# Optimization experiments

Hardware: AMD Instinct MI355X
Metric: run time of the kernel (lower is better)

## Reference

```python
import jax, jax.numpy as jnp
import numpy as np

B, C, H, W = 32, 256, 56, 56
HEADS, M, EXP = 8, 7, 4


def _rel_pos_index(m):
    # Swin V1 pair-wise relative position index, [m*m, m*m] (static)
    coords = np.stack(np.meshgrid(np.arange(m), np.arange(m), indexing='ij'))  # [2,m,m]
    cf = coords.reshape(2, -1)
    rel = (cf[:, :, None] - cf[:, None, :]).transpose(1, 2, 0).copy()
    rel[:, :, 0] += m - 1
    rel[:, :, 1] += m - 1
    rel[:, :, 0] *= 2 * m - 1
    return jnp.asarray(rel.sum(-1))


def setup_inputs():
    key = jax.random.key(0)
    ks = jax.random.split(key, 8)
    s = lambda k, shp: jax.random.normal(k, shp, jnp.float32) * 0.02
    return {
        'x': jax.random.normal(ks[0], (B, C, H, W), jnp.float32),
        'qkv_w': s(ks[1], (3 * C, C)), 'qkv_b': jnp.zeros((3 * C,), jnp.float32),
        'proj_w': s(ks[2], (C, C)), 'proj_b': jnp.zeros((C,), jnp.float32),
        'bias_table': s(ks[3], ((2 * M - 1) * (2 * M - 1), HEADS)),
        'ln1_g': jnp.ones((C,), jnp.float32), 'ln1_b': jnp.zeros((C,), jnp.float32),
        'ln2_g': jnp.ones((C,), jnp.float32), 'ln2_b': jnp.zeros((C,), jnp.float32),
        'w1': s(ks[4], (EXP * C, C)), 'b1': jnp.zeros((EXP * C,), jnp.float32),
        'w2': s(ks[5], (C, EXP * C)), 'b2': jnp.zeros((C,), jnp.float32),
    }


def _layernorm(x, g, b, eps=1e-5):
    mu = x.mean(-1, keepdims=True)
    var = ((x - mu) ** 2).mean(-1, keepdims=True)
    return (x - mu) * jax.lax.rsqrt(var + eps) * g + b


def _block(x, qkv_w, qkv_b, proj_w, proj_b, bias_table,
           ln1_g, ln1_b, ln2_g, ln2_b, w1, b1, w2, b2):
    Bx, Cx, Hx, Wx = x.shape
    N = M * M
    # window partition: [B,C,H,W] -> [B*nw, M*M, C]
    xp = x.reshape(Bx, Cx, Hx // M, M, Wx // M, M)
    xp = xp.transpose(0, 2, 4, 3, 5, 1).reshape(-1, N, Cx)
    B_ = xp.shape[0]
    # relative self-attention (pre-LN)
    h = _layernorm(xp, ln1_g, ln1_b)
    qkv = (h @ qkv_w.T + qkv_b).reshape(B_, N, 3, HEADS, Cx // HEADS)
    qkv = qkv.transpose(2, 0, 3, 1, 4)  # [3,B_,H,N,d]
    q, k, v = qkv[0], qkv[1], qkv[2]
    q = q * (HEADS ** -0.5)  # note: module scales by num_heads**-0.5 (faithful)
    rel_idx = _rel_pos_index(M)
    bias = bias_table[rel_idx.reshape(-1)].reshape(N, N, HEADS).transpose(2, 0, 1)
    attn = jax.nn.softmax(jnp.einsum('bhnd,bhmd->bhnm', q, k) + bias[None], axis=-1)
    out = jnp.einsum('bhnm,bhmd->bhnd', attn, v).transpose(0, 2, 1, 3).reshape(B_, N, Cx)
    xp = xp + (out @ proj_w.T + proj_b)
    # MLP (1x1 Conv1d == pointwise linear), exact GELU as in torch
    h2 = _layernorm(xp, ln2_g, ln2_b)
    h2 = jax.nn.gelu(h2 @ w1.T + b1, approximate=False)
    xp = xp + (h2 @ w2.T + b2)
    # window reverse: [B*nw, M*M, C] -> [B,C,H,W]
    nwh, nww = Hx // M, Wx // M
    y = xp.reshape(Bx, nwh, nww, M, M, Cx).transpose(0, 5, 1, 3, 2, 4).reshape(Bx, Cx, Hx, Wx)
    return y


def reference(x, qkv_w, qkv_b, proj_w, proj_b, bias_table,
              ln1_g, ln1_b, ln2_g, ln2_b, w1, b1, w2, b2):
    return _block(x, qkv_w, qkv_b, proj_w, proj_b, bias_table,
                  ln1_g, ln1_b, ln2_g, ln2_b, w1, b1, w2, b2)
```

## Files before the change

kernel.cpp:

```cpp
#include <hip/hip_runtime.h>
#include <math.h>

#define TB 256

typedef short bf16x8 __attribute__((ext_vector_type(8)));
typedef short s16x4 __attribute__((ext_vector_type(4)));
typedef float f32x4 __attribute__((ext_vector_type(4)));
typedef unsigned short u16;

__device__ __forceinline__ float b2f(u16 u){
  union{unsigned i; float f;} v; v.i=((unsigned)u)<<16; return v.f;
}
__device__ __forceinline__ u16 f2b(float f){
  union{float ff; unsigned i;} v; v.ff=f;
  return (u16)((v.i + 0x7FFFu + ((v.i>>16)&1u))>>16);
}

__device__ __forceinline__ float gelu(float x){
  float z = fabsf(x)*0.70710678118654752f;
  float t = 1.0f/fmaf(0.3275911f, z, 1.0f);
  float p = t*fmaf(t, fmaf(t, fmaf(t, fmaf(t, 1.061405429f, -1.453152027f), 1.421413741f), -0.284496736f), 0.254829592f);
  float erfz = fmaf(-p, __expf(-z*z), 1.0f);
  float s = (x >= 0.f) ? erfz : -erfz;
  return 0.5f*x*(1.0f + s);
}

__global__ void k_prep(const float* __restrict__ qkv_w, const float* __restrict__ proj_w,
                       const float* __restrict__ w1, const float* __restrict__ w2,
                       const float* __restrict__ btab,
                       u16* __restrict__ wq, u16* __restrict__ wp,
                       u16* __restrict__ w1b, u16* __restrict__ w2b,
                       float* __restrict__ biasT){
  int i = blockIdx.x*TB + threadIdx.x;
  if(i < 196608){ wq[i] = f2b(qkv_w[i]); return; }
  i -= 196608;
  if(i < 65536){ wp[i] = f2b(proj_w[i]); return; }
  i -= 65536;
  if(i < 262144){ w1b[i] = f2b(w1[i]); return; }
  i -= 262144;
  if(i < 262144){ w2b[i] = f2b(w2[i]); return; }
  i -= 262144;
  if(i < 32768){
    int h = i>>12, kq = i&4095, k = kq>>6, q = kq&63;
    float v = 0.f;
    if(k<49 && q<49){
      int qi=q/7, qj=q-qi*7, ki=k/7, kj=k-ki*7;
      v = btab[((qi-ki+6)*13 + (qj-kj+6))*8 + h];
    }
    biasT[i] = v;
  }
}

__global__ __launch_bounds__(256) void k_post(const u16* __restrict__ x2lin, float* __restrict__ out){
  __shared__ u16 tile[12544];
  const int bid = blockIdx.x;
  const int bb = bid>>6, wh=(bid>>3)&7, chunk=bid&7;
  const int wb = bb*64 + wh*8;
  for(int e=threadIdx.x; e<12544; e+=256){
    int ww = e/1568, rem = e - ww*1568, r = rem>>5, cc = rem&31;
    tile[cc*392 + ww*49 + r] = x2lin[(size_t)(wb+ww)*12544 + r*256 + chunk*32 + cc];
  }
  __syncthreads();
  for(int idx=threadIdx.x; idx<12544; idx+=256){
    int c = idx/392, rem = idx - c*392, ii = rem/56, w = rem - ii*56;
    int ww = w/7, j = w - ww*7;
    out[((size_t)(bb*256 + chunk*32 + c))*3136 + (size_t)(wh*7+ii)*56 + w]
        = b2f(tile[c*392 + ww*49 + ii*7 + j]);
  }
}

#define QB_OFF  32768
#define KB_OFF  65536
#define VT_OFF  98304
#define XS_OFF  65536
#define BLK_LDS 131072

__global__ __launch_bounds__(1024,2) void k_block(
    const float* __restrict__ x,
    const u16* __restrict__ wqkv,  const float* __restrict__ bqkv,
    const u16* __restrict__ wproj, const float* __restrict__ bproj,
    const float* __restrict__ biasT,
    const float* __restrict__ g1, const float* __restrict__ bt1,
    const u16* __restrict__ w1, const float* __restrict__ b1v,
    const u16* __restrict__ w2, const float* __restrict__ b2v,
    const float* __restrict__ g2, const float* __restrict__ bt2,
    u16* __restrict__ x2lin)
{
  extern __shared__ char lds[];
  const int tid = threadIdx.x;
  const int wv = tid >> 6, l = tid & 63;
  const int lr = l & 15, lg = l >> 4;
  const unsigned swzA = ((unsigned)(lr & 7)) << 4;
  const unsigned swzR = ((unsigned)((lr>>2) & 3)) << 4;
  const int win = ((blockIdx.x & 7) << 8) | (blockIdx.x >> 3);
  const int bb = win >> 6, wh = (win >> 3) & 7, ww = win & 7;
  const float* xwin = x + (size_t)bb*802816 + (size_t)wh*392 + ww*7;

  float* xs = (float*)(lds + XS_OFF);
  {
    const int j = tid & 7, rbase = tid >> 3;
    #pragma unroll
    for(int it=0; it<14; ++it){
      int run = it*128 + rbase;
      int c = run/7, ii = run - (run/7)*7;
      if(j<7) xs[c*53 + ii*7 + j] = xwin[(size_t)c*3136 + ii*56 + j];
    }
  }
  __syncthreads();

  {
    float gg[4], bgm[4];
    #pragma unroll
    for(int k2=0;k2<4;++k2){ gg[k2]=g1[l+64*k2]; bgm[k2]=bt1[l+64*k2]; }
    #pragma unroll
    for(int s=0;s<4;++s){
      int n = wv + s*16;
      if(n<49){
        float xv[4];
        #pragma unroll
        for(int k2=0;k2<4;++k2) xv[k2] = xs[(l+64*k2)*53 + n];
        float sm=0.f, sq=0.f;
        #pragma unroll
        for(int k2=0;k2<4;++k2){ sm+=xv[k2]; sq+=xv[k2]*xv[k2]; }
        #pragma unroll
        for(int off=32;off>=1;off>>=1){ sm+=__shfl_xor(sm,off); sq+=__shfl_xor(sq,off); }
        float mu=sm*(1.f/256.f), var=sq*(1.f/256.f)-mu*mu;
        float rs=rsqrtf(var+1e-5f);
        #pragma unroll
        for(int k2=0;k2<4;++k2){
          int c=l+64*k2;
          unsigned off2 = (((unsigned)n)*512u + ((unsigned)c)*2u) ^ (((unsigned)(n&7))<<4);
          *(u16*)(lds + off2) = f2b((xv[k2]-mu)*rs*gg[k2]+bgm[k2]);
        }
      }
    }
  }
  for(int m=tid; m<3840; m+=1024) *(u16*)(lds + 49*512 + m*2) = 0;
  __syncthreads();

  for(int m=tid; m<3840; m+=1024){
    int hd = m/480, rm = m - hd*480;
    int d = rm/15, r = 49 + (rm - (rm/15)*15);
    *(u16*)(lds + ((unsigned)(VT_OFF + hd*4096 + d*128 + r*2) ^ ((((unsigned)d)&7u)<<4))) = 0;
  }

  for(int ct=wv; ct<48; ct+=16){
    const u16* wrow = wqkv + ((size_t)(ct*16+lr))*256 + lg*8;
    f32x4 acc[4];
    #pragma unroll
    for(int rt=0;rt<4;++rt) acc[rt]=(f32x4){0.f,0.f,0.f,0.f};
    #pragma unroll
    for(int kq=0; kq<4; ++kq){
      bf16x8 bfr[2];
      #pragma unroll
      for(int k=0;k<2;++k) bfr[k] = *(const bf16x8*)(wrow + kq*64 + k*32);
      #pragma unroll
      for(int rt=0; rt<4; ++rt){
        #pragma unroll
        for(int k=0;k<2;++k){
          bf16x8 afr = *(const bf16x8*)(lds + ((((unsigned)(rt*16+lr))*512u + (unsigned)((kq*2+k)*64+lg*16)) ^ swzA));
          acc[rt] = __builtin_amdgcn_mfma_f32_16x16x32_bf16(bfr[k], afr, acc[rt], 0,0,0);
        }
      }
    }
    f32x4 b4 = *(const f32x4*)(bqkv + ct*16 + lg*4);
    const int s3 = ct>>4, hd = (ct>>1)&7, db = (ct&1)*16 + lg*4;
    #pragma unroll
    for(int rt=0; rt<4; ++rt){
      const int r = rt*16 + lr;
      if(r<49){
        if(s3==0){
          s16x4 pk;
          #pragma unroll
          for(int i=0;i<4;++i) pk[i] = (short)f2b((acc[rt][i]+b4[i])*0.35355339059327373f);
          *(s16x4*)(lds + ((unsigned)(QB_OFF + hd*4096 + r*64 + db*2) ^ swzR)) = pk;
        } else if(s3==1){
          s16x4 pk;
          #pragma unroll
          for(int i=0;i<4;++i) pk[i] = (short)f2b(acc[rt][i]+b4[i]);
          *(s16x4*)(lds + ((unsigned)(KB_OFF + hd*4096 + r*64 + db*2) ^ swzR)) = pk;
        } else {
          #pragma unroll
          for(int i=0;i<4;++i)
            *(u16*)(lds + ((unsigned)(VT_OFF + hd*4096 + (db+i)*128 + r*2) ^ ((((unsigned)(db+i))&7u)<<4))) = f2b(acc[rt][i]+b4[i]);
        }
      }
    }
  }
  __syncthreads();

  {
    const int h = wv & 7, half = wv >> 3;
    s16x4 pkk[2][4];
    #pragma unroll
    for(int j=0;j<2;++j){
      const int qt = half*2 + j;
      bf16x8 qf = *(const bf16x8*)(lds + ((unsigned)(QB_OFF + h*4096 + (qt*16+lr)*64 + lg*16) ^ swzR));
      f32x4 st[4];
      #pragma unroll
      for(int kt=0;kt<4;++kt){
        bf16x8 kfk = *(const bf16x8*)(lds + ((unsigned)(KB_OFF + h*4096 + (kt*16+lr)*64 + lg*16) ^ swzR));
        f32x4 bini;
        #pragma unroll
        for(int i=0;i<4;++i) bini[i] = biasT[h*4096 + (kt*16+lg*4+i)*64 + qt*16+lr];
        st[kt] = __builtin_amdgcn_mfma_f32_16x16x32_bf16(kfk, qf, bini, 0,0,0);
      }
      #pragma unroll
      for(int i=0;i<4;++i)
        if(!(lg==0 && i==0)) st[3][i] = -1e30f;

      float mx = -1e30f;
      #pragma unroll
      for(int kt=0;kt<4;++kt)
        #pragma unroll
        for(int i=0;i<4;++i) mx = fmaxf(mx, st[kt][i]);
      mx = fmaxf(mx, __shfl_xor(mx,16));
      mx = fmaxf(mx, __shfl_xor(mx,32));
      float su = 0.f;
      #pragma unroll
      for(int kt=0;kt<4;++kt)
        #pragma unroll
        for(int i=0;i<4;++i){ float p = __expf(st[kt][i]-mx); st[kt][i]=p; su+=p; }
      su += __shfl_xor(su,16);
      su += __shfl_xor(su,32);
      float inv = 1.f/su;
      #pragma unroll
      for(int kt=0;kt<4;++kt)
        #pragma unroll
        for(int i=0;i<4;++i) pkk[j][kt][i] = (short)f2b(st[kt][i]*inv);
    }
    __syncthreads();

    char* Pb = lds + h*8192;
    #pragma unroll
    for(int j=0;j<2;++j){
      const unsigned rq = (unsigned)((half*2+j)*16 + lr);
      #pragma unroll
      for(int kt=0;kt<4;++kt)
        *(s16x4*)(Pb + ((rq*128u + (unsigned)(kt*32+lg*8)) ^ swzA)) = pkk[j][kt];
    }
    #pragma unroll
    for(int j=0;j<2;++j){
      const int qt = half*2 + j;
      const unsigned rq = (unsigned)(qt*16 + lr);
      bf16x8 pf0 = *(const bf16x8*)(Pb + ((rq*128u + (unsigned)(lg*16)) ^ swzA));
      bf16x8 pf1 = *(const bf16x8*)(Pb + ((rq*128u + (unsigned)(64+lg*16)) ^ swzA));
      #pragma unroll
      for(int dt=0;dt<2;++dt){
        bf16x8 vf0 = *(const bf16x8*)(lds + ((unsigned)(VT_OFF + h*4096 + (dt*16+lr)*128 + lg*16) ^ swzA));
        bf16x8 vf1 = *(const bf16x8*)(lds + ((unsigned)(VT_OFF + h*4096 + (dt*16+lr)*128 + 64+lg*16) ^ swzA));
        f32x4 o = {0.f,0.f,0.f,0.f};
        o = __builtin_amdgcn_mfma_f32_16x16x32_bf16(pf0, vf0, o, 0,0,0);
        o = __builtin_amdgcn_mfma_f32_16x16x32_bf16(pf1, vf1, o, 0,0,0);
        #pragma unroll
        for(int i=0;i<4;++i)
          *(u16*)(lds + ((unsigned)(KB_OFF + h*4096 + (qt*16+lg*4+i)*64 + (dt*16+lr)*2) ^ (((unsigned)lg)<<4))) = f2b(o[i]);
      }
    }
  }
  __syncthreads();

  {
    const int c = wv*16 + lr;
    const u16* wrow = wproj + (size_t)c*256 + lg*8;
    const float pbP = bproj[c];
    f32x4 acc[4];
    #pragma unroll
    for(int mt=0;mt<4;++mt) acc[mt]=(f32x4){0.f,0.f,0.f,0.f};
    #pragma unroll
    for(int kq=0; kq<4; ++kq){
      bf16x8 bfrP[2];
      #pragma unroll
      for(int k=0;k<2;++k) bfrP[k] = *(const bf16x8*)(wrow + kq*64 + k*32);
      #pragma unroll
      for(int mt=0; mt<4; ++mt){
        #pragma unroll
        for(int k=0;k<2;++k){
          bf16x8 afr = *(const bf16x8*)(lds + ((unsigned)(KB_OFF + (kq*2+k)*4096 + (mt*16+lr)*64 + lg*16) ^ swzR));
          acc[mt] = __builtin_amdgcn_mfma_f32_16x16x32_bf16(afr, bfrP[k], acc[mt], 0,0,0);
        }
      }
    }
    #pragma unroll
    for(int mt=0; mt<4; ++mt){
      #pragma unroll
      for(int i=0;i<4;++i){
        int r = mt*16 + lg*4 + i;
        if(r<49){
          int ii=r/7, jj=r-ii*7;
          float val = acc[mt][i] + pbP + xwin[(size_t)c*3136 + ii*56 + jj];
          *(u16*)(lds + ((((unsigned)r)*512u + ((unsigned)c)*2u) ^ (((unsigned)(r&7))<<4))) = f2b(val);
        }
      }
    }
  }
  for(int m=tid; m<3840; m+=1024){
    int r = 49 + (m>>8), c = m & 255;
    *(u16*)(lds + ((((unsigned)r)*512u + ((unsigned)c)*2u) ^ (((unsigned)(r&7))<<4))) = 0;
  }
  __syncthreads();

  {
    float gg[4], bb2[4];
    #pragma unroll
    for(int k2=0;k2<4;++k2){ gg[k2]=g2[l+64*k2]; bb2[k2]=bt2[l+64*k2]; }
    #pragma unroll
    for(int rr=0; rr<4; ++rr){
      int r = wv*4 + rr;
      float v[4];
      #pragma unroll
      for(int k2=0;k2<4;++k2)
        v[k2] = b2f(*(const u16*)(lds + ((((unsigned)r)*512u + ((unsigned)(l+64*k2))*2u) ^ (((unsigned)(r&7))<<4))));
      float sm=v[0]+v[1]+v[2]+v[3];
      float sq=v[0]*v[0]+v[1]*v[1]+v[2]*v[2]+v[3]*v[3];
      #pragma unroll
      for(int off=32;off>=1;off>>=1){ sm+=__shfl_xor(sm,off); sq+=__shfl_xor(sq,off); }
      float mu=sm*(1.f/256.f), var=sq*(1.f/256.f)-mu*mu, rs=rsqrtf(var+1e-5f);
      #pragma unroll
      for(int k2=0;k2<4;++k2){
        int c=l+64*k2;
        unsigned off2 = 32768u + ((((unsigned)r)*512u + ((unsigned)c)*2u) ^ (((unsigned)(r&7))<<4));
        *(u16*)(lds + off2) = f2b((v[k2]-mu)*rs*gg[k2]+bb2[k2]);
      }
    }
  }
  __syncthreads();

  const int hcol = wv*16 + lr;
  f32x4 acc2[4];
  #pragma unroll
  for(int mt=0;mt<4;++mt) acc2[mt]=(f32x4){0.f,0.f,0.f,0.f};

  {
    const u16* wrow = w1 + (size_t)hcol*256 + lg*8;
    const float bias1 = b1v[hcol];
    f32x4 acc[4];
    #pragma unroll
    for(int mt=0;mt<4;++mt) acc[mt]=(f32x4){0.f,0.f,0.f,0.f};
    #pragma unroll
    for(int kq=0; kq<4; ++kq){
      bf16x8 bfr1[2];
      #pragma unroll
      for(int k=0;k<2;++k) bfr1[k] = *(const bf16x8*)(wrow + kq*64 + k*32);
      #pragma unroll
      for(int mt=0; mt<4; ++mt){
        #pragma unroll
        for(int k=0;k<2;++k){
          bf16x8 afr = *(const bf16x8*)(lds + 32768u + ((((unsigned)(mt*16+lr))*512u + (unsigned)((kq*2+k)*64+lg*16)) ^ swzA));
          acc[mt] = __builtin_amdgcn_mfma_f32_16x16x32_bf16(afr, bfr1[k], acc[mt], 0,0,0);
        }
      }
    }
    #pragma unroll
    for(int mt=0; mt<4; ++mt)
      #pragma unroll
      for(int i2=0;i2<4;++i2){
        int r = mt*16 + lg*4 + i2;
        *(u16*)(lds + 98304u + ((((unsigned)r)*512u + ((unsigned)hcol)*2u) ^ (((unsigned)(r&7))<<4))) = f2b(gelu(acc[mt][i2]+bias1));
      }
  }
  __syncthreads();

  for(int kc=0; kc<4; ++kc){
    if(kc<3){
      const int gcol = (kc+1)*256 + hcol;
      const u16* wrow = w1 + (size_t)gcol*256 + lg*8;
      const float biasN = b1v[gcol];
      const unsigned dst = ((kc+1)&1) ? 65536u : 98304u;
      f32x4 acc[4];
      #pragma unroll
      for(int mt=0;mt<4;++mt) acc[mt]=(f32x4){0.f,0.f,0.f,0.f};
      #pragma unroll
      for(int kq=0; kq<4; ++kq){
        bf16x8 bfrN[2];
        #pragma unroll
        for(int k=0;k<2;++k) bfrN[k] = *(const bf16x8*)(wrow + kq*64 + k*32);
        #pragma unroll
        for(int mt=0; mt<4; ++mt){
          #pragma unroll
          for(int k=0;k<2;++k){
            bf16x8 afr = *(const bf16x8*)(lds + 32768u + ((((unsigned)(mt*16+lr))*512u + (unsigned)((kq*2+k)*64+lg*16)) ^ swzA));
            acc[mt] = __builtin_amdgcn_mfma_f32_16x16x32_bf16(afr, bfrN[k], acc[mt], 0,0,0);
          }
        }
      }
      #pragma unroll
      for(int mt=0; mt<4; ++mt)
        #pragma unroll
        for(int i2=0;i2<4;++i2){
          int r = mt*16 + lg*4 + i2;
          *(u16*)(lds + dst + ((((unsigned)r)*512u + ((unsigned)hcol)*2u) ^ (((unsigned)(r&7))<<4))) = f2b(gelu(acc[mt][i2]+biasN));
        }
    }
    {
      const u16* wrow = w2 + (size_t)hcol*1024 + kc*256 + lg*8;
      const unsigned src = (kc&1) ? 65536u : 98304u;
      __builtin_amdgcn_s_setprio(1);
      #pragma unroll
      for(int kq=0; kq<4; ++kq){
        bf16x8 bfr2[2];
        #pragma unroll
        for(int k=0;k<2;++k) bfr2[k] = *(const bf16x8*)(wrow + kq*64 + k*32);
        #pragma unroll
        for(int mt=0; mt<4; ++mt){
          #pragma unroll
          for(int k=0;k<2;++k){
            bf16x8 afr = *(const bf16x8*)(lds + src + ((((unsigned)(mt*16+lr))*512u + (unsigned)((kq*2+k)*64+lg*16)) ^ swzA));
            acc2[mt] = __builtin_amdgcn_mfma_f32_16x16x32_bf16(afr, bfr2[k], acc2[mt], 0,0,0);
          }
        }
      }
      __builtin_amdgcn_s_setprio(0);
    }
    __syncthreads();
  }

  {
    const int c = hcol;
    const float biasc = b2v[c];
    #pragma unroll
    for(int mt=0; mt<4; ++mt){
      #pragma unroll
      for(int i2=0;i2<4;++i2){
        int r = mt*16 + lg*4 + i2;
        float resid = b2f(*(const u16*)(lds + ((((unsigned)r)*512u + ((unsigned)c)*2u) ^ (((unsigned)(r&7))<<4))));
        float val = acc2[mt][i2] + biasc + resid;
        *(float*)(lds + 32768u + ((((unsigned)r)*1024u + ((unsigned)c)*4u) ^ ((((unsigned)(r>>2))&3u)<<6))) = val;
      }
    }
  }
  __syncthreads();

  for(int u=tid; u<12544; u+=1024){
    int r = u>>8, c = u&255;
    float v = *(const float*)(lds + 32768u + ((((unsigned)r)*1024u + ((unsigned)c)*4u) ^ ((((unsigned)(r>>2))&3u)<<6)));
    x2lin[(size_t)win*12544 + u] = f2b(v);
  }
}

extern "C" void kernel_launch(void* const* d_in, const int* in_sizes, int n_in,
                              void* d_out, int out_size, void* d_ws, size_t ws_size,
                              hipStream_t stream) {
  const float* x      = (const float*)d_in[0];
  const float* qkv_w  = (const float*)d_in[1];
  const float* qkv_b  = (const float*)d_in[2];
  const float* proj_w = (const float*)d_in[3];
  const float* proj_b = (const float*)d_in[4];
  const float* btab   = (const float*)d_in[5];
  const float* ln1g   = (const float*)d_in[6];
  const float* ln1b   = (const float*)d_in[7];
  const float* ln2g   = (const float*)d_in[8];
  const float* ln2b   = (const float*)d_in[9];
  const float* w1     = (const float*)d_in[10];
  const float* b1     = (const float*)d_in[11];
  const float* w2     = (const float*)d_in[12];
  const float* b2     = (const float*)d_in[13];

  char* ws = (char*)d_ws;
  float* biasT = (float*)ws;
  u16*   wq    = (u16*)(ws + 131072);
  u16*   wp    = (u16*)(ws + 524288);
  u16*   w1b   = (u16*)(ws + 655360);
  u16*   w2b   = (u16*)(ws + 1179648);
  u16*   x2l   = (u16*)(ws + 1703936);

  k_prep<<<3200, TB, 0, stream>>>(qkv_w, proj_w, w1, w2, btab, wq, wp, w1b, w2b, biasT);

  hipFuncSetAttribute((const void*)k_block, hipFuncAttributeMaxDynamicSharedMemorySize, BLK_LDS);
  k_block<<<2048, 1024, BLK_LDS, stream>>>(x, wq, qkv_b, wp, proj_b, biasT, ln1g, ln1b,
                                           w1b, b1, w2b, b2, ln2g, ln2b, x2l);
  k_post<<<2048, 256, 0, stream>>>(x2l, (float*)d_out);
}
```

Before: 745.4 us.

## Split fused window block into separate attention and MLP kernels

Splits the single fused attention+MLP kernel into two kernels: attention writes its residual output to a global bf16 buffer (reusing the output allocation as scratch), and a separate MLP kernel reads it back, applies LN2, the MLP and the residual. The MLP kernel needs less LDS (96KB vs 128KB) and both use launch_bounds(1024,4), aiming to lower register pressure and raise occupancy in each phase. In exchange it adds a global round-trip of the intermediate activations and an extra launch, and the residual is reread from global memory.

```diff
diff --git a/kernel.cpp b/kernel.cpp
--- a/kernel.cpp
+++ b/kernel.cpp
@@ -73,18 +73,15 @@
 #define KB_OFF  65536
 #define VT_OFF  98304
 #define XS_OFF  65536
-#define BLK_LDS 131072
-
-__global__ __launch_bounds__(1024,2) void k_block(
+#define ATT_LDS 131072
+
+__global__ __launch_bounds__(1024,4) void k_attn(
     const float* __restrict__ x,
     const u16* __restrict__ wqkv,  const float* __restrict__ bqkv,
     const u16* __restrict__ wproj, const float* __restrict__ bproj,
     const float* __restrict__ biasT,
     const float* __restrict__ g1, const float* __restrict__ bt1,
-    const u16* __restrict__ w1, const float* __restrict__ b1v,
-    const u16* __restrict__ w2, const float* __restrict__ b2v,
-    const float* __restrict__ g2, const float* __restrict__ bt2,
-    u16* __restrict__ x2lin)
+    u16* __restrict__ xtbuf)
 {
   extern __shared__ char lds[];
   const int tid = threadIdx.x;
@@ -294,35 +291,59 @@
       }
     }
   }
+  __syncthreads();
+
+  for(int u=tid; u<12544; u+=1024){
+    int r = u>>8, c = u&255;
+    xtbuf[(size_t)win*12544 + u] = *(const u16*)(lds + ((((unsigned)r)*512u + ((unsigned)c)*2u) ^ (((unsigned)(r&7))<<4)));
+  }
+}
+
+#define MLP_LDS 98304
+
+__global__ __launch_bounds__(1024,4) void k_mlp(
+    const u16* __restrict__ xtbuf,
+    const u16* __restrict__ w1, const float* __restrict__ b1v,
+    const u16* __restrict__ w2, const float* __restrict__ b2v,
+    const float* __restrict__ g2, const float* __restrict__ bt2,
+    u16* __restrict__ x2lin)
+{
+  extern __shared__ char lds[];
+  const int tid = threadIdx.x;
+  const int wv = tid >> 6, l = tid & 63;
+  const int lr = l & 15, lg = l >> 4;
+  const unsigned swzA = ((unsigned)(lr & 7)) << 4;
+  const int win = ((blockIdx.x & 7) << 8) | (blockIdx.x >> 3);
+  const size_t base = (size_t)win*12544;
+
+  {
+    float gg[4], bb2[4];
+    #pragma unroll
+    for(int k2=0;k2<4;++k2){ gg[k2]=g2[l+64*k2]; bb2[k2]=bt2[l+64*k2]; }
+    #pragma unroll
+    for(int rr=0; rr<4; ++rr){
+      int r = wv*4 + rr;
+      if(r<49){
+        float v[4];
+        #pragma unroll
+        for(int k2=0;k2<4;++k2) v[k2] = b2f(xtbuf[base + r*256 + l + 64*k2]);
+        float sm=v[0]+v[1]+v[2]+v[3];
+        float sq=v[0]*v[0]+v[1]*v[1]+v[2]*v[2]+v[3]*v[3];
+        #pragma unroll
+        for(int off=32;off>=1;off>>=1){ sm+=__shfl_xor(sm,off); sq+=__shfl_xor(sq,off); }
+        float mu=sm*(1.f/256.f), var=sq*(1.f/256.f)-mu*mu, rs=rsqrtf(var+1e-5f);
+        #pragma unroll
+        for(int k2=0;k2<4;++k2){
+          int c=l+64*k2;
+          unsigned off2 = (((unsigned)r)*512u + ((unsigned)c)*2u) ^ (((unsigned)(r&7))<<4);
+          *(u16*)(lds + off2) = f2b((v[k2]-mu)*rs*gg[k2]+bb2[k2]);
+        }
+      }
+    }
+  }
   for(int m=tid; m<3840; m+=1024){
     int r = 49 + (m>>8), c = m & 255;
     *(u16*)(lds + ((((unsigned)r)*512u + ((unsigned)c)*2u) ^ (((unsigned)(r&7))<<4))) = 0;
-  }
-  __syncthreads();
-
-  {
-    float gg[4], bb2[4];
-    #pragma unroll
-    for(int k2=0;k2<4;++k2){ gg[k2]=g2[l+64*k2]; bb2[k2]=bt2[l+64*k2]; }
-    #pragma unroll
-    for(int rr=0; rr<4; ++rr){
-      int r = wv*4 + rr;
-      float v[4];
-      #pragma unroll
-      for(int k2=0;k2<4;++k2)
-        v[k2] = b2f(*(const u16*)(lds + ((((unsigned)r)*512u + ((unsigned)(l+64*k2))*2u) ^ (((unsigned)(r&7))<<4))));
-      float sm=v[0]+v[1]+v[2]+v[3];
-      float sq=v[0]*v[0]+v[1]*v[1]+v[2]*v[2]+v[3]*v[3];
-      #pragma unroll
-      for(int off=32;off>=1;off>>=1){ sm+=__shfl_xor(sm,off); sq+=__shfl_xor(sq,off); }
-      float mu=sm*(1.f/256.f), var=sq*(1.f/256.f)-mu*mu, rs=rsqrtf(var+1e-5f);
-      #pragma unroll
-      for(int k2=0;k2<4;++k2){
-        int c=l+64*k2;
-        unsigned off2 = 32768u + ((((unsigned)r)*512u + ((unsigned)c)*2u) ^ (((unsigned)(r&7))<<4));
-        *(u16*)(lds + off2) = f2b((v[k2]-mu)*rs*gg[k2]+bb2[k2]);
-      }
-    }
   }
   __syncthreads();
 
@@ -346,7 +367,7 @@
       for(int mt=0; mt<4; ++mt){
         #pragma unroll
         for(int k=0;k<2;++k){
-          bf16x8 afr = *(const bf16x8*)(lds + 32768u + ((((unsigned)(mt*16+lr))*512u + (unsigned)((kq*2+k)*64+lg*16)) ^ swzA));
+          bf16x8 afr = *(const bf16x8*)(lds + ((((unsigned)(mt*16+lr))*512u + (unsigned)((kq*2+k)*64+lg*16)) ^ swzA));
           acc[mt] = __builtin_amdgcn_mfma_f32_16x16x32_bf16(afr, bfr1[k], acc[mt], 0,0,0);
         }
       }
@@ -356,7 +377,7 @@
       #pragma unroll
       for(int i2=0;i2<4;++i2){
         int r = mt*16 + lg*4 + i2;
-        *(u16*)(lds + 98304u + ((((unsigned)r)*512u + ((unsigned)hcol)*2u) ^ (((unsigned)(r&7))<<4))) = f2b(gelu(acc[mt][i2]+bias1));
+        *(u16*)(lds + 32768u + ((((unsigned)r)*512u + ((unsigned)hcol)*2u) ^ (((unsigned)(r&7))<<4))) = f2b(gelu(acc[mt][i2]+bias1));
       }
   }
   __syncthreads();
@@ -366,7 +387,7 @@
       const int gcol = (kc+1)*256 + hcol;
       const u16* wrow = w1 + (size_t)gcol*256 + lg*8;
       const float biasN = b1v[gcol];
-      const unsigned dst = ((kc+1)&1) ? 65536u : 98304u;
+      const unsigned dst = ((kc+1)&1) ? 65536u : 32768u;
       f32x4 acc[4];
       #pragma unroll
       for(int mt=0;mt<4;++mt) acc[mt]=(f32x4){0.f,0.f,0.f,0.f};
@@ -379,7 +400,7 @@
         for(int mt=0; mt<4; ++mt){
           #pragma unroll
           for(int k=0;k<2;++k){
-            bf16x8 afr = *(const bf16x8*)(lds + 32768u + ((((unsigned)(mt*16+lr))*512u + (unsigned)((kq*2+k)*64+lg*16)) ^ swzA));
+            bf16x8 afr = *(const bf16x8*)(lds + ((((unsigned)(mt*16+lr))*512u + (unsigned)((kq*2+k)*64+lg*16)) ^ swzA));
             acc[mt] = __builtin_amdgcn_mfma_f32_16x16x32_bf16(afr, bfrN[k], acc[mt], 0,0,0);
           }
         }
@@ -394,7 +415,7 @@
     }
     {
       const u16* wrow = w2 + (size_t)hcol*1024 + kc*256 + lg*8;
-      const unsigned src = (kc&1) ? 65536u : 98304u;
+      const unsigned src = (kc&1) ? 65536u : 32768u;
       __builtin_amdgcn_s_setprio(1);
       #pragma unroll
       for(int kq=0; kq<4; ++kq){
@@ -415,6 +436,7 @@
     __syncthreads();
   }
 
+  u16* fin = (u16*)(lds + 32768);
   {
     const int c = hcol;
     const float biasc = b2v[c];
@@ -423,19 +445,17 @@
       #pragma unroll
       for(int i2=0;i2<4;++i2){
         int r = mt*16 + lg*4 + i2;
-        float resid = b2f(*(const u16*)(lds + ((((unsigned)r)*512u + ((unsigned)c)*2u) ^ (((unsigned)(r&7))<<4))));
-        float val = acc2[mt][i2] + biasc + resid;
-        *(float*)(lds + 32768u + ((((unsigned)r)*1024u + ((unsigned)c)*4u) ^ ((((unsigned)(r>>2))&3u)<<6))) = val;
-      }
-    }
-  }
-  __syncthreads();
-
-  for(int u=tid; u<12544; u+=1024){
-    int r = u>>8, c = u&255;
-    float v = *(const float*)(lds + 32768u + ((((unsigned)r)*1024u + ((unsigned)c)*4u) ^ ((((unsigned)(r>>2))&3u)<<6)));
-    x2lin[(size_t)win*12544 + u] = f2b(v);
-  }
+        if(r<49){
+          float resid = b2f(xtbuf[base + r*256 + c]);
+          fin[r*256 + c] = f2b(acc2[mt][i2] + biasc + resid);
+        }
+      }
+    }
+  }
+  __syncthreads();
+
+  for(int u=tid; u<12544; u+=1024)
+    x2lin[base + u] = fin[u];
 }
 
 extern "C" void kernel_launch(void* const* d_in, const int* in_sizes, int n_in,
@@ -463,11 +483,13 @@
   u16*   w1b   = (u16*)(ws + 655360);
   u16*   w2b   = (u16*)(ws + 1179648);
   u16*   x2l   = (u16*)(ws + 1703936);
+  u16*   xtb   = (u16*)d_out;
 
   k_prep<<<3200, TB, 0, stream>>>(qkv_w, proj_w, w1, w2, btab, wq, wp, w1b, w2b, biasT);
 
-  hipFuncSetAttribute((const void*)k_block, hipFuncAttributeMaxDynamicSharedMemorySize, BLK_LDS);
-  k_block<<<2048, 1024, BLK_LDS, stream>>>(x, wq, qkv_b, wp, proj_b, biasT, ln1g, ln1b,
-                                           w1b, b1, w2b, b2, ln2g, ln2b, x2l);
+  hipFuncSetAttribute((const void*)k_attn, hipFuncAttributeMaxDynamicSharedMemorySize, ATT_LDS);
+  hipFuncSetAttribute((const void*)k_mlp,  hipFuncAttributeMaxDynamicSharedMemorySize, MLP_LDS);
+  k_attn<<<2048, 1024, ATT_LDS, stream>>>(x, wq, qkv_b, wp, proj_b, biasT, ln1g, ln1b, xtb);
+  k_mlp <<<2048, 1024, MLP_LDS, stream>>>(xtb, w1b, b1, w2b, b2, ln2g, ln2b, x2l);
   k_post<<<2048, 256, 0, stream>>>(x2l, (float*)d_out);
 }
```

Result: faster. 714.6 us (-4.1%).
